# Performance work log

Measured on AMD Instinct MI355X. Metric: run time of the kernel, lower is better.

Reference implementation:

```python
import jax, jax.numpy as jnp
import numpy as np

N, M, B, L, D = 100000, 256, 8, 128, 64
COORD_MAX = 1024


def setup_inputs() -> dict:
    key = jax.random.key(0)
    ks = jax.random.split(key, 9)
    # batch ids sorted so the original loop's centroid_offset == column index
    clu_b = jnp.sort(jax.random.randint(ks[0], (N, 1), 0, B))
    cen_b = jnp.sort(jax.random.randint(ks[1], (M, 1), 0, B))
    clu_xyz = jax.random.randint(ks[2], (N, 3), 0, COORD_MAX)
    cen_xyz = jax.random.randint(ks[3], (M, 3), 0, COORD_MAX)
    return {
        "cluster_coords": jnp.concatenate([clu_b, clu_xyz], axis=1).astype(jnp.int32),
        "centroid_coords": jnp.concatenate([cen_b, cen_xyz], axis=1).astype(jnp.int32),
        "cluster_feats": jax.random.normal(ks[4], (N, L), jnp.float32),
        "centroid_feats": jax.random.normal(ks[5], (M, L), jnp.float32),
        "centroid_conf": jax.random.uniform(ks[6], (M, 1), jnp.float32),
        "W": jax.random.normal(ks[7], (L, D), jnp.float32) * 0.05,
        "b": jax.random.normal(ks[8], (D,), jnp.float32) * 0.05,
    }


def reference(cluster_coords, centroid_coords, cluster_feats, centroid_feats,
              centroid_conf, W, b):
    # pointwise Conv3d(k=1) == linear on features
    clu = cluster_feats @ W + b                      # [N, D]
    nrm = jnp.maximum(jnp.linalg.norm(clu, axis=1, keepdims=True), 1e-12)
    clu = clu / nrm                                  # F.normalize(p=2, dim=1)
    cen = centroid_conf * (centroid_feats @ W + b)   # [M, D]

    # same-batch mask replaces the python loop + scatter
    valid = cluster_coords[:, 0][:, None] == centroid_coords[:, 0][None, :]  # [N, M]

    # pairwise L2 distance on spatial coords via squared expansion (exact for small ints)
    cc = cluster_coords[:, 1:].astype(jnp.float32)   # [N, 3]
    ec = centroid_coords[:, 1:].astype(jnp.float32)  # [M, 3]
    d2 = (jnp.sum(cc * cc, axis=1)[:, None]
          + jnp.sum(ec * ec, axis=1)[None, :]
          - 2.0 * cc @ ec.T)
    dist = jnp.maximum(jnp.sqrt(jnp.maximum(d2, 0.0)), 0.1)  # clamp(min=0.1)

    logits = jnp.where(valid, -dist, -jnp.inf)
    attn = jax.nn.softmax(logits, axis=-1)           # per-row over same-batch centroids
    attn = jnp.where(valid, attn, 0.0)               # rows w/ no centroids -> 0 (matches zeros init)

    out = (clu @ cen.T) * attn                       # [N, M]
    return out
```

## Files before the change

kernel.cpp:

```cpp
#include <hip/hip_runtime.h>
#include <stdint.h>


#define NN 100000
#define MM 256
#define LL 128
#define DD 64
#define NTILES (NN / 16)

typedef float f32x4 __attribute__((ext_vector_type(4)));
typedef __bf16 bf16x8 __attribute__((ext_vector_type(8)));
typedef __fp16 fp16x2 __attribute__((ext_vector_type(2)));

union U16x8 { uint4 u; bf16x8 v; unsigned short s[8]; };
union UH2 { unsigned int u; fp16x2 h; };

static __device__ __forceinline__ unsigned short f2bf(float f) {
  union { float f; unsigned int i; } t; t.f = f;
  unsigned int x = t.i;
  x += 0x7fffu + ((x >> 16) & 1u);
  return (unsigned short)(x >> 16);
}

__global__ __launch_bounds__(256) void prep_kernel(
    const int* __restrict__ cen_coords,
    const float* __restrict__ cen_feats,
    const float* __restrict__ conf,
    const float* __restrict__ W,
    const float* __restrict__ bvec,
    unsigned short* __restrict__ cen_ws,
    unsigned short* __restrict__ wt_ws,
    float4* __restrict__ cmeta_ws)
{
  int tid = threadIdx.x;
  if (blockIdx.x < 16) {
    int m = blockIdx.x * 16 + (tid >> 4);
    int c = tid & 15;
    float a0 = 0.f, a1 = 0.f, a2 = 0.f, a3 = 0.f;
    for (int l = 0; l < LL; l++) {
      float f = cen_feats[m * LL + l];
      const float* wr = W + l * DD + c;
      a0 += f * wr[0];  a1 += f * wr[16];
      a2 += f * wr[32]; a3 += f * wr[48];
    }
    float cf = conf[m];
    cen_ws[m * DD + c +  0] = f2bf(cf * (a0 + bvec[c +  0]));
    cen_ws[m * DD + c + 16] = f2bf(cf * (a1 + bvec[c + 16]));
    cen_ws[m * DD + c + 32] = f2bf(cf * (a2 + bvec[c + 32]));
    cen_ws[m * DD + c + 48] = f2bf(cf * (a3 + bvec[c + 48]));
  } else {
    for (int i = tid; i < LL * DD; i += 256) {
      int l = i >> 6, d = i & 63;
      wt_ws[d * LL + l] = f2bf(W[l * DD + d]);
    }
    {
      int4 cc = ((const int4*)cen_coords)[tid];
      float4 f;
      f.x = (float)cc.y + 4096.0f * (float)cc.x;
      f.y = (float)cc.z;
      f.z = (float)cc.w;
      f.w = 0.0f;
      cmeta_ws[tid] = f;
    }
  }
}

__global__ __launch_bounds__(256, 4) void main_kernel(
    const int4* __restrict__ clu_coords4,
    const float* __restrict__ feats,
    const float* __restrict__ bvec,
    const unsigned short* __restrict__ cen_ws,
    const unsigned short* __restrict__ wt_ws,
    const float4* __restrict__ cmeta,
    float* __restrict__ out)
{
  __shared__ __align__(16) unsigned short clu_s[4][16 * 72];

  int tid = threadIdx.x;
  int wave = tid >> 6, lane = tid & 63;
  int q = lane >> 4, c = lane & 15;
  int tile = blockIdx.x * 4 + wave;
  if (tile >= NTILES) return;

  const float4* fb = (const float4*)(feats + (size_t)(tile * 16 + c) * LL);
  float4 ff[8];
#pragma unroll
  for (int ks = 0; ks < 4; ks++) {
    ff[2 * ks]     = fb[ks * 8 + q * 2];
    ff[2 * ks + 1] = fb[ks * 8 + q * 2 + 1];
  }
  float rx[4], ry[4], rz[4];
#pragma unroll
  for (int r = 0; r < 4; r++) {
    int4 rm = clu_coords4[tile * 16 + q * 4 + r];
    rx[r] = (float)rm.y + 4096.0f * (float)rm.x;
    ry[r] = (float)rm.z;
    rz[r] = (float)rm.w;
  }

  float d2m[4] = {1e30f, 1e30f, 1e30f, 1e30f};
#pragma unroll 4
  for (int mt = 0; mt < 16; mt++) {
    float4 cm = cmeta[mt * 16 + c];
#pragma unroll
    for (int r = 0; r < 4; r++) {
      float dx = rx[r] - cm.x, dy = ry[r] - cm.y, dz = rz[r] - cm.z;
      d2m[r] = fminf(d2m[r], dx * dx + dy * dy + dz * dz);
    }
  }
  float dmv[4];
#pragma unroll
  for (int r = 0; r < 4; r++) {
    d2m[r] = fminf(d2m[r], __shfl_xor(d2m[r], 1));
    d2m[r] = fminf(d2m[r], __shfl_xor(d2m[r], 2));
    d2m[r] = fminf(d2m[r], __shfl_xor(d2m[r], 4));
    d2m[r] = fminf(d2m[r], __shfl_xor(d2m[r], 8));
    dmv[r] = fmaxf(sqrtf(d2m[r]), 0.1f);
  }

  uint2 ep[16];
  float rsum[4] = {0.f, 0.f, 0.f, 0.f};
#pragma unroll
  for (int mt = 0; mt < 16; mt++) {
    float4 cm = cmeta[mt * 16 + c];
    float e[4];
#pragma unroll
    for (int r = 0; r < 4; r++) {
      float dx = rx[r] - cm.x, dy = ry[r] - cm.y, dz = rz[r] - cm.z;
      float d = fmaxf(sqrtf(dx * dx + dy * dy + dz * dz), 0.1f);
      e[r] = __expf(dmv[r] - d);
      rsum[r] += e[r];
    }
    UH2 p0, p1;
    p0.h = __builtin_amdgcn_cvt_pkrtz(e[0], e[1]);
    p1.h = __builtin_amdgcn_cvt_pkrtz(e[2], e[3]);
    ep[mt].x = p0.u;
    ep[mt].y = p1.u;
  }
  float sc[4];
#pragma unroll
  for (int r = 0; r < 4; r++) {
    rsum[r] += __shfl_xor(rsum[r], 1);
    rsum[r] += __shfl_xor(rsum[r], 2);
    rsum[r] += __shfl_xor(rsum[r], 4);
    rsum[r] += __shfl_xor(rsum[r], 8);
    sc[r] = (d2m[r] < 4.0e6f) ? 1.0f / rsum[r] : 0.f;
  }

  f32x4 acc[4] = {{0,0,0,0},{0,0,0,0},{0,0,0,0},{0,0,0,0}};
  {
    const uint4* wb = (const uint4*)wt_ws;
#pragma unroll
    for (int ks = 0; ks < 4; ks++) {
      float4 f0 = ff[2 * ks], f1 = ff[2 * ks + 1];
      U16x8 a;
      a.v[0] = (__bf16)f0.x; a.v[1] = (__bf16)f0.y; a.v[2] = (__bf16)f0.z; a.v[3] = (__bf16)f0.w;
      a.v[4] = (__bf16)f1.x; a.v[5] = (__bf16)f1.y; a.v[6] = (__bf16)f1.z; a.v[7] = (__bf16)f1.w;
#pragma unroll
      for (int nt = 0; nt < 4; nt++) {
        U16x8 b; b.u = wb[(nt * 16 + c) * 16 + ks * 4 + q];
        acc[nt] = __builtin_amdgcn_mfma_f32_16x16x32_bf16(a.v, b.v, acc[nt], 0, 0, 0);
      }
    }
  }
#pragma unroll
  for (int nt = 0; nt < 4; nt++) {
    float bv = bvec[nt * 16 + c];
    acc[nt][0] += bv; acc[nt][1] += bv; acc[nt][2] += bv; acc[nt][3] += bv;
  }
  float inv_nrm[4];
#pragma unroll
  for (int r = 0; r < 4; r++) {
    float s = acc[0][r]*acc[0][r] + acc[1][r]*acc[1][r] + acc[2][r]*acc[2][r] + acc[3][r]*acc[3][r];
    s += __shfl_xor(s, 1); s += __shfl_xor(s, 2); s += __shfl_xor(s, 4); s += __shfl_xor(s, 8);
    inv_nrm[r] = 1.0f / fmaxf(sqrtf(s), 1e-12f);
  }
#pragma unroll
  for (int nt = 0; nt < 4; nt++)
#pragma unroll
    for (int r = 0; r < 4; r++) {
      union { __bf16 h; unsigned short s; } u;
      u.h = (__bf16)(acc[nt][r] * inv_nrm[r]);
      clu_s[wave][(q * 4 + r) * 72 + nt * 16 + c] = u.s;
    }

  __builtin_amdgcn_sched_barrier(0);

  const uint4* cb = (const uint4*)(clu_s[wave]);
  U16x8 a0, a1;
  a0.u = cb[c * 9 + q];
  a1.u = cb[c * 9 + 4 + q];

  const uint4* cenb = (const uint4*)cen_ws;
  float* ob = out + (size_t)(tile * 16 + q * 4) * MM + c;
#pragma unroll
  for (int mt = 0; mt < 16; mt++) {
    U16x8 b0, b1;
    b0.u = cenb[(mt * 16 + c) * 8 + q];
    b1.u = cenb[(mt * 16 + c) * 8 + 4 + q];
    f32x4 dacc = {0, 0, 0, 0};
    dacc = __builtin_amdgcn_mfma_f32_16x16x32_bf16(a0.v, b0.v, dacc, 0, 0, 0);
    dacc = __builtin_amdgcn_mfma_f32_16x16x32_bf16(a1.v, b1.v, dacc, 0, 0, 0);
    UH2 p0, p1; p0.u = ep[mt].x; p1.u = ep[mt].y;
    ob[0 * MM + mt * 16] = dacc[0] * ((float)p0.h[0] * sc[0]);
    ob[1 * MM + mt * 16] = dacc[1] * ((float)p0.h[1] * sc[1]);
    ob[2 * MM + mt * 16] = dacc[2] * ((float)p1.h[0] * sc[2]);
    ob[3 * MM + mt * 16] = dacc[3] * ((float)p1.h[1] * sc[3]);
  }
}

extern "C" void kernel_launch(void* const* d_in, const int* in_sizes, int n_in,
                              void* d_out, int out_size, void* d_ws, size_t ws_size,
                              hipStream_t stream) {
  const int* clu_coords = (const int*)d_in[0];
  const int* cen_coords = (const int*)d_in[1];
  const float* clu_feats = (const float*)d_in[2];
  const float* cen_feats = (const float*)d_in[3];
  const float* conf      = (const float*)d_in[4];
  const float* W         = (const float*)d_in[5];
  const float* bvec      = (const float*)d_in[6];
  float* out = (float*)d_out;

  char* ws = (char*)d_ws;
  unsigned short* cen_ws = (unsigned short*)ws;
  unsigned short* wt_ws  = (unsigned short*)(ws + 32768);
  float4* cmeta_ws       = (float4*)(ws + 32768 + 16384);

  prep_kernel<<<17, 256, 0, stream>>>(cen_coords, cen_feats, conf, W, bvec,
                                      cen_ws, wt_ws, cmeta_ws);
  main_kernel<<<(NTILES + 3) / 4, 256, 0, stream>>>(
      (const int4*)clu_coords, clu_feats, bvec, cen_ws, wt_ws, cmeta_ws, out);
}
```

Measured before the change: 209.0 us.

## Process two row tiles per wave with prefetch and LDS-staged centroid metadata

Each wave now handles two consecutive 16-row tiles. It prefetches the second tile's feature rows right after the first tile's projection MFMAs, so that load overlaps the softmax and output work. Centroid coordinate metadata is staged once per block in shared memory instead of being re-read from global memory in the distance loops. The launch-bounds occupancy hint is dropped and the grid halves, which lowers parallelism and may raise register pressure. Output is written exactly as before.

```diff
diff --git a/kernel.cpp b/kernel.cpp
--- a/kernel.cpp
+++ b/kernel.cpp
@@ -7,6 +7,7 @@
 #define LL 128
 #define DD 64
 #define NTILES (NN / 16)
+#define NJOBS (NTILES / 2)
 
 typedef float f32x4 __attribute__((ext_vector_type(4)));
 typedef __bf16 bf16x8 __attribute__((ext_vector_type(8)));
@@ -65,7 +66,7 @@
   }
 }
 
-__global__ __launch_bounds__(256, 4) void main_kernel(
+__global__ __launch_bounds__(256) void main_kernel(
     const int4* __restrict__ clu_coords4,
     const float* __restrict__ feats,
     const float* __restrict__ bvec,
@@ -75,137 +76,161 @@
     float* __restrict__ out)
 {
   __shared__ __align__(16) unsigned short clu_s[4][16 * 72];
+  __shared__ __align__(16) float4 cmeta_s[MM];
 
   int tid = threadIdx.x;
+  cmeta_s[tid] = cmeta[tid];
+  __syncthreads();
+
   int wave = tid >> 6, lane = tid & 63;
   int q = lane >> 4, c = lane & 15;
-  int tile = blockIdx.x * 4 + wave;
-  if (tile >= NTILES) return;
-
-  const float4* fb = (const float4*)(feats + (size_t)(tile * 16 + c) * LL);
+  int job = blockIdx.x * 4 + wave;
+  if (job >= NJOBS) return;
+  int tile0 = job * 2;
+
+  const float4* fb = (const float4*)(feats + (size_t)(tile0 * 16 + c) * LL);
   float4 ff[8];
 #pragma unroll
   for (int ks = 0; ks < 4; ks++) {
     ff[2 * ks]     = fb[ks * 8 + q * 2];
     ff[2 * ks + 1] = fb[ks * 8 + q * 2 + 1];
   }
-  float rx[4], ry[4], rz[4];
-#pragma unroll
-  for (int r = 0; r < 4; r++) {
-    int4 rm = clu_coords4[tile * 16 + q * 4 + r];
-    rx[r] = (float)rm.y + 4096.0f * (float)rm.x;
-    ry[r] = (float)rm.z;
-    rz[r] = (float)rm.w;
-  }
-
-  float d2m[4] = {1e30f, 1e30f, 1e30f, 1e30f};
+
+#pragma unroll
+  for (int tt = 0; tt < 2; tt++) {
+    int tile = tile0 + tt;
+
+    int4 rm[4];
+#pragma unroll
+    for (int r = 0; r < 4; r++)
+      rm[r] = clu_coords4[tile * 16 + q * 4 + r];
+
+    f32x4 acc[4] = {{0,0,0,0},{0,0,0,0},{0,0,0,0},{0,0,0,0}};
+    {
+      const uint4* wb = (const uint4*)wt_ws;
+#pragma unroll
+      for (int ks = 0; ks < 4; ks++) {
+        float4 f0 = ff[2 * ks], f1 = ff[2 * ks + 1];
+        U16x8 a;
+        a.v[0] = (__bf16)f0.x; a.v[1] = (__bf16)f0.y; a.v[2] = (__bf16)f0.z; a.v[3] = (__bf16)f0.w;
+        a.v[4] = (__bf16)f1.x; a.v[5] = (__bf16)f1.y; a.v[6] = (__bf16)f1.z; a.v[7] = (__bf16)f1.w;
+#pragma unroll
+        for (int nt = 0; nt < 4; nt++) {
+          U16x8 b; b.u = wb[(nt * 16 + c) * 16 + ks * 4 + q];
+          acc[nt] = __builtin_amdgcn_mfma_f32_16x16x32_bf16(a.v, b.v, acc[nt], 0, 0, 0);
+        }
+      }
+    }
+
+    if (tt == 0) {
+#pragma unroll
+      for (int ks = 0; ks < 4; ks++) {
+        ff[2 * ks]     = fb[512 + ks * 8 + q * 2];
+        ff[2 * ks + 1] = fb[512 + ks * 8 + q * 2 + 1];
+      }
+    }
+
+#pragma unroll
+    for (int nt = 0; nt < 4; nt++) {
+      float bv = bvec[nt * 16 + c];
+      acc[nt][0] += bv; acc[nt][1] += bv; acc[nt][2] += bv; acc[nt][3] += bv;
+    }
+    float inv_nrm[4];
+#pragma unroll
+    for (int r = 0; r < 4; r++) {
+      float s = acc[0][r]*acc[0][r] + acc[1][r]*acc[1][r] + acc[2][r]*acc[2][r] + acc[3][r]*acc[3][r];
+      s += __shfl_xor(s, 1); s += __shfl_xor(s, 2); s += __shfl_xor(s, 4); s += __shfl_xor(s, 8);
+      inv_nrm[r] = 1.0f / fmaxf(sqrtf(s), 1e-12f);
+    }
+#pragma unroll
+    for (int nt = 0; nt < 4; nt++)
+#pragma unroll
+      for (int r = 0; r < 4; r++) {
+        union { __bf16 h; unsigned short s; } u;
+        u.h = (__bf16)(acc[nt][r] * inv_nrm[r]);
+        clu_s[wave][(q * 4 + r) * 72 + nt * 16 + c] = u.s;
+      }
+
+    __builtin_amdgcn_sched_barrier(0);
+
+    const uint4* cb = (const uint4*)(clu_s[wave]);
+    U16x8 a0, a1;
+    a0.u = cb[c * 9 + q];
+    a1.u = cb[c * 9 + 4 + q];
+
+    float rx[4], ry[4], rz[4];
+#pragma unroll
+    for (int r = 0; r < 4; r++) {
+      rx[r] = (float)rm[r].y + 4096.0f * (float)rm[r].x;
+      ry[r] = (float)rm[r].z;
+      rz[r] = (float)rm[r].w;
+    }
+
+    float d2m[4] = {1e30f, 1e30f, 1e30f, 1e30f};
 #pragma unroll 4
-  for (int mt = 0; mt < 16; mt++) {
-    float4 cm = cmeta[mt * 16 + c];
-#pragma unroll
-    for (int r = 0; r < 4; r++) {
-      float dx = rx[r] - cm.x, dy = ry[r] - cm.y, dz = rz[r] - cm.z;
-      d2m[r] = fminf(d2m[r], dx * dx + dy * dy + dz * dz);
-    }
-  }
-  float dmv[4];
-#pragma unroll
-  for (int r = 0; r < 4; r++) {
-    d2m[r] = fminf(d2m[r], __shfl_xor(d2m[r], 1));
-    d2m[r] = fminf(d2m[r], __shfl_xor(d2m[r], 2));
-    d2m[r] = fminf(d2m[r], __shfl_xor(d2m[r], 4));
-    d2m[r] = fminf(d2m[r], __shfl_xor(d2m[r], 8));
-    dmv[r] = fmaxf(sqrtf(d2m[r]), 0.1f);
-  }
-
-  uint2 ep[16];
-  float rsum[4] = {0.f, 0.f, 0.f, 0.f};
-#pragma unroll
-  for (int mt = 0; mt < 16; mt++) {
-    float4 cm = cmeta[mt * 16 + c];
-    float e[4];
-#pragma unroll
-    for (int r = 0; r < 4; r++) {
-      float dx = rx[r] - cm.x, dy = ry[r] - cm.y, dz = rz[r] - cm.z;
-      float d = fmaxf(sqrtf(dx * dx + dy * dy + dz * dz), 0.1f);
-      e[r] = __expf(dmv[r] - d);
-      rsum[r] += e[r];
-    }
-    UH2 p0, p1;
-    p0.h = __builtin_amdgcn_cvt_pkrtz(e[0], e[1]);
-    p1.h = __builtin_amdgcn_cvt_pkrtz(e[2], e[3]);
-    ep[mt].x = p0.u;
-    ep[mt].y = p1.u;
-  }
-  float sc[4];
-#pragma unroll
-  for (int r = 0; r < 4; r++) {
-    rsum[r] += __shfl_xor(rsum[r], 1);
-    rsum[r] += __shfl_xor(rsum[r], 2);
-    rsum[r] += __shfl_xor(rsum[r], 4);
-    rsum[r] += __shfl_xor(rsum[r], 8);
-    sc[r] = (d2m[r] < 4.0e6f) ? 1.0f / rsum[r] : 0.f;
-  }
-
-  f32x4 acc[4] = {{0,0,0,0},{0,0,0,0},{0,0,0,0},{0,0,0,0}};
-  {
-    const uint4* wb = (const uint4*)wt_ws;
-#pragma unroll
-    for (int ks = 0; ks < 4; ks++) {
-      float4 f0 = ff[2 * ks], f1 = ff[2 * ks + 1];
-      U16x8 a;
-      a.v[0] = (__bf16)f0.x; a.v[1] = (__bf16)f0.y; a.v[2] = (__bf16)f0.z; a.v[3] = (__bf16)f0.w;
-      a.v[4] = (__bf16)f1.x; a.v[5] = (__bf16)f1.y; a.v[6] = (__bf16)f1.z; a.v[7] = (__bf16)f1.w;
-#pragma unroll
-      for (int nt = 0; nt < 4; nt++) {
-        U16x8 b; b.u = wb[(nt * 16 + c) * 16 + ks * 4 + q];
-        acc[nt] = __builtin_amdgcn_mfma_f32_16x16x32_bf16(a.v, b.v, acc[nt], 0, 0, 0);
-      }
-    }
-  }
-#pragma unroll
-  for (int nt = 0; nt < 4; nt++) {
-    float bv = bvec[nt * 16 + c];
-    acc[nt][0] += bv; acc[nt][1] += bv; acc[nt][2] += bv; acc[nt][3] += bv;
-  }
-  float inv_nrm[4];
-#pragma unroll
-  for (int r = 0; r < 4; r++) {
-    float s = acc[0][r]*acc[0][r] + acc[1][r]*acc[1][r] + acc[2][r]*acc[2][r] + acc[3][r]*acc[3][r];
-    s += __shfl_xor(s, 1); s += __shfl_xor(s, 2); s += __shfl_xor(s, 4); s += __shfl_xor(s, 8);
-    inv_nrm[r] = 1.0f / fmaxf(sqrtf(s), 1e-12f);
-  }
-#pragma unroll
-  for (int nt = 0; nt < 4; nt++)
-#pragma unroll
-    for (int r = 0; r < 4; r++) {
-      union { __bf16 h; unsigned short s; } u;
-      u.h = (__bf16)(acc[nt][r] * inv_nrm[r]);
-      clu_s[wave][(q * 4 + r) * 72 + nt * 16 + c] = u.s;
-    }
-
-  __builtin_amdgcn_sched_barrier(0);
-
-  const uint4* cb = (const uint4*)(clu_s[wave]);
-  U16x8 a0, a1;
-  a0.u = cb[c * 9 + q];
-  a1.u = cb[c * 9 + 4 + q];
-
-  const uint4* cenb = (const uint4*)cen_ws;
-  float* ob = out + (size_t)(tile * 16 + q * 4) * MM + c;
-#pragma unroll
-  for (int mt = 0; mt < 16; mt++) {
-    U16x8 b0, b1;
-    b0.u = cenb[(mt * 16 + c) * 8 + q];
-    b1.u = cenb[(mt * 16 + c) * 8 + 4 + q];
-    f32x4 dacc = {0, 0, 0, 0};
-    dacc = __builtin_amdgcn_mfma_f32_16x16x32_bf16(a0.v, b0.v, dacc, 0, 0, 0);
-    dacc = __builtin_amdgcn_mfma_f32_16x16x32_bf16(a1.v, b1.v, dacc, 0, 0, 0);
-    UH2 p0, p1; p0.u = ep[mt].x; p1.u = ep[mt].y;
-    ob[0 * MM + mt * 16] = dacc[0] * ((float)p0.h[0] * sc[0]);
-    ob[1 * MM + mt * 16] = dacc[1] * ((float)p0.h[1] * sc[1]);
-    ob[2 * MM + mt * 16] = dacc[2] * ((float)p1.h[0] * sc[2]);
-    ob[3 * MM + mt * 16] = dacc[3] * ((float)p1.h[1] * sc[3]);
+    for (int mt = 0; mt < 16; mt++) {
+      float4 cm = cmeta_s[mt * 16 + c];
+#pragma unroll
+      for (int r = 0; r < 4; r++) {
+        float dx = rx[r] - cm.x, dy = ry[r] - cm.y, dz = rz[r] - cm.z;
+        d2m[r] = fminf(d2m[r], dx * dx + dy * dy + dz * dz);
+      }
+    }
+    float dmv[4];
+#pragma unroll
+    for (int r = 0; r < 4; r++) {
+      d2m[r] = fminf(d2m[r], __shfl_xor(d2m[r], 1));
+      d2m[r] = fminf(d2m[r], __shfl_xor(d2m[r], 2));
+      d2m[r] = fminf(d2m[r], __shfl_xor(d2m[r], 4));
+      d2m[r] = fminf(d2m[r], __shfl_xor(d2m[r], 8));
+      dmv[r] = fmaxf(sqrtf(d2m[r]), 0.1f);
+    }
+
+    uint2 ep[16];
+    float rsum[4] = {0.f, 0.f, 0.f, 0.f};
+#pragma unroll
+    for (int mt = 0; mt < 16; mt++) {
+      float4 cm = cmeta_s[mt * 16 + c];
+      float e[4];
+#pragma unroll
+      for (int r = 0; r < 4; r++) {
+        float dx = rx[r] - cm.x, dy = ry[r] - cm.y, dz = rz[r] - cm.z;
+        float d = fmaxf(sqrtf(dx * dx + dy * dy + dz * dz), 0.1f);
+        e[r] = __expf(dmv[r] - d);
+        rsum[r] += e[r];
+      }
+      UH2 p0, p1;
+      p0.h = __builtin_amdgcn_cvt_pkrtz(e[0], e[1]);
+      p1.h = __builtin_amdgcn_cvt_pkrtz(e[2], e[3]);
+      ep[mt].x = p0.u;
+      ep[mt].y = p1.u;
+    }
+    float sc[4];
+#pragma unroll
+    for (int r = 0; r < 4; r++) {
+      rsum[r] += __shfl_xor(rsum[r], 1);
+      rsum[r] += __shfl_xor(rsum[r], 2);
+      rsum[r] += __shfl_xor(rsum[r], 4);
+      rsum[r] += __shfl_xor(rsum[r], 8);
+      sc[r] = (d2m[r] < 4.0e6f) ? 1.0f / rsum[r] : 0.f;
+    }
+
+    const uint4* cenb = (const uint4*)cen_ws;
+    float* ob = out + (size_t)(tile * 16 + q * 4) * MM + c;
+#pragma unroll
+    for (int mt = 0; mt < 16; mt++) {
+      U16x8 b0, b1;
+      b0.u = cenb[(mt * 16 + c) * 8 + q];
+      b1.u = cenb[(mt * 16 + c) * 8 + 4 + q];
+      f32x4 dacc = {0, 0, 0, 0};
+      dacc = __builtin_amdgcn_mfma_f32_16x16x32_bf16(a0.v, b0.v, dacc, 0, 0, 0);
+      dacc = __builtin_amdgcn_mfma_f32_16x16x32_bf16(a1.v, b1.v, dacc, 0, 0, 0);
+      UH2 p0, p1; p0.u = ep[mt].x; p1.u = ep[mt].y;
+      ob[0 * MM + mt * 16] = dacc[0] * ((float)p0.h[0] * sc[0]);
+      ob[1 * MM + mt * 16] = dacc[1] * ((float)p0.h[1] * sc[1]);
+      ob[2 * MM + mt * 16] = dacc[2] * ((float)p1.h[0] * sc[2]);
+      ob[3 * MM + mt * 16] = dacc[3] * ((float)p1.h[1] * sc[3]);
+    }
   }
 }
 
@@ -228,6 +253,6 @@
 
   prep_kernel<<<17, 256, 0, stream>>>(cen_coords, cen_feats, conf, W, bvec,
                                       cen_ws, wt_ws, cmeta_ws);
-  main_kernel<<<(NTILES + 3) / 4, 256, 0, stream>>>(
+  main_kernel<<<(NJOBS + 3) / 4, 256, 0, stream>>>(
       (const int4*)clu_coords, clu_feats, bvec, cen_ws, wt_ws, cmeta_ws, out);
 }
```

Measured after the change: 202.6 us. 1.03x faster.

## Transpose MFMA output mapping for float4 row stores and stage centroid meta in LDS

Applied to the files above, without the earlier changes.

Swaps the MFMA operand order so each lane holds four consecutive centroid columns of a single cluster row. This turns the output writes into float4 stores, and the attention math becomes one row per lane, reducing shuffles and per-row state. Centroid metadata is staged once into shared memory with a block barrier, and the linear/normalize stage is moved ahead of the distance computation. Occupancy hint is raised from 4 to 5 blocks per CU, which may cause register spills.

```diff
diff --git a/kernel.cpp b/kernel.cpp
--- a/kernel.cpp
+++ b/kernel.cpp
@@ -65,7 +65,7 @@
   }
 }
 
-__global__ __launch_bounds__(256, 4) void main_kernel(
+__global__ __launch_bounds__(256, 5) void main_kernel(
     const int4* __restrict__ clu_coords4,
     const float* __restrict__ feats,
     const float* __restrict__ bvec,
@@ -75,8 +75,12 @@
     float* __restrict__ out)
 {
   __shared__ __align__(16) unsigned short clu_s[4][16 * 72];
+  __shared__ __align__(16) float4 cmeta_s[MM];
 
   int tid = threadIdx.x;
+  cmeta_s[tid] = cmeta[tid];
+  __syncthreads();
+
   int wave = tid >> 6, lane = tid & 63;
   int q = lane >> 4, c = lane & 15;
   int tile = blockIdx.x * 4 + wave;
@@ -89,47 +93,81 @@
     ff[2 * ks]     = fb[ks * 8 + q * 2];
     ff[2 * ks + 1] = fb[ks * 8 + q * 2 + 1];
   }
-  float rx[4], ry[4], rz[4];
+  int4 rm = clu_coords4[tile * 16 + c];
+  float rx = (float)rm.y + 4096.0f * (float)rm.x;
+  float ry = (float)rm.z;
+  float rz = (float)rm.w;
+
+  f32x4 acc[4] = {{0,0,0,0},{0,0,0,0},{0,0,0,0},{0,0,0,0}};
+  {
+    const uint4* wb = (const uint4*)wt_ws;
+#pragma unroll
+    for (int ks = 0; ks < 4; ks++) {
+      float4 f0 = ff[2 * ks], f1 = ff[2 * ks + 1];
+      U16x8 a;
+      a.v[0] = (__bf16)f0.x; a.v[1] = (__bf16)f0.y; a.v[2] = (__bf16)f0.z; a.v[3] = (__bf16)f0.w;
+      a.v[4] = (__bf16)f1.x; a.v[5] = (__bf16)f1.y; a.v[6] = (__bf16)f1.z; a.v[7] = (__bf16)f1.w;
+#pragma unroll
+      for (int nt = 0; nt < 4; nt++) {
+        U16x8 b; b.u = wb[(nt * 16 + c) * 16 + ks * 4 + q];
+        acc[nt] = __builtin_amdgcn_mfma_f32_16x16x32_bf16(a.v, b.v, acc[nt], 0, 0, 0);
+      }
+    }
+  }
+#pragma unroll
+  for (int nt = 0; nt < 4; nt++) {
+    float bv = bvec[nt * 16 + c];
+    acc[nt][0] += bv; acc[nt][1] += bv; acc[nt][2] += bv; acc[nt][3] += bv;
+  }
+  float inv_nrm[4];
 #pragma unroll
   for (int r = 0; r < 4; r++) {
-    int4 rm = clu_coords4[tile * 16 + q * 4 + r];
-    rx[r] = (float)rm.y + 4096.0f * (float)rm.x;
-    ry[r] = (float)rm.z;
-    rz[r] = (float)rm.w;
-  }
-
-  float d2m[4] = {1e30f, 1e30f, 1e30f, 1e30f};
-#pragma unroll 4
+    float s = acc[0][r]*acc[0][r] + acc[1][r]*acc[1][r] + acc[2][r]*acc[2][r] + acc[3][r]*acc[3][r];
+    s += __shfl_xor(s, 1); s += __shfl_xor(s, 2); s += __shfl_xor(s, 4); s += __shfl_xor(s, 8);
+    inv_nrm[r] = 1.0f / fmaxf(sqrtf(s), 1e-12f);
+  }
+#pragma unroll
+  for (int nt = 0; nt < 4; nt++)
+#pragma unroll
+    for (int r = 0; r < 4; r++) {
+      union { __bf16 h; unsigned short s; } u;
+      u.h = (__bf16)(acc[nt][r] * inv_nrm[r]);
+      clu_s[wave][(q * 4 + r) * 72 + nt * 16 + c] = u.s;
+    }
+
+  __builtin_amdgcn_sched_barrier(0);
+
+  const uint4* cb = (const uint4*)(clu_s[wave]);
+  U16x8 a0, a1;
+  a0.u = cb[c * 9 + q];
+  a1.u = cb[c * 9 + 4 + q];
+
+  float d2m = 1e30f;
+#pragma unroll
   for (int mt = 0; mt < 16; mt++) {
-    float4 cm = cmeta[mt * 16 + c];
 #pragma unroll
     for (int r = 0; r < 4; r++) {
-      float dx = rx[r] - cm.x, dy = ry[r] - cm.y, dz = rz[r] - cm.z;
-      d2m[r] = fminf(d2m[r], dx * dx + dy * dy + dz * dz);
-    }
-  }
-  float dmv[4];
-#pragma unroll
-  for (int r = 0; r < 4; r++) {
-    d2m[r] = fminf(d2m[r], __shfl_xor(d2m[r], 1));
-    d2m[r] = fminf(d2m[r], __shfl_xor(d2m[r], 2));
-    d2m[r] = fminf(d2m[r], __shfl_xor(d2m[r], 4));
-    d2m[r] = fminf(d2m[r], __shfl_xor(d2m[r], 8));
-    dmv[r] = fmaxf(sqrtf(d2m[r]), 0.1f);
-  }
+      float4 cm = cmeta_s[mt * 16 + q * 4 + r];
+      float dx = rx - cm.x, dy = ry - cm.y, dz = rz - cm.z;
+      d2m = fminf(d2m, dx * dx + dy * dy + dz * dz);
+    }
+  }
+  d2m = fminf(d2m, __shfl_xor(d2m, 16));
+  d2m = fminf(d2m, __shfl_xor(d2m, 32));
+  float dmv = fmaxf(sqrtf(d2m), 0.1f);
 
   uint2 ep[16];
-  float rsum[4] = {0.f, 0.f, 0.f, 0.f};
+  float rsum = 0.f;
 #pragma unroll
   for (int mt = 0; mt < 16; mt++) {
-    float4 cm = cmeta[mt * 16 + c];
     float e[4];
 #pragma unroll
     for (int r = 0; r < 4; r++) {
-      float dx = rx[r] - cm.x, dy = ry[r] - cm.y, dz = rz[r] - cm.z;
+      float4 cm = cmeta_s[mt * 16 + q * 4 + r];
+      float dx = rx - cm.x, dy = ry - cm.y, dz = rz - cm.z;
       float d = fmaxf(sqrtf(dx * dx + dy * dy + dz * dz), 0.1f);
-      e[r] = __expf(dmv[r] - d);
-      rsum[r] += e[r];
+      e[r] = __expf(dmv - d);
+      rsum += e[r];
     }
     UH2 p0, p1;
     p0.h = __builtin_amdgcn_cvt_pkrtz(e[0], e[1]);
@@ -137,75 +175,27 @@
     ep[mt].x = p0.u;
     ep[mt].y = p1.u;
   }
-  float sc[4];
-#pragma unroll
-  for (int r = 0; r < 4; r++) {
-    rsum[r] += __shfl_xor(rsum[r], 1);
-    rsum[r] += __shfl_xor(rsum[r], 2);
-    rsum[r] += __shfl_xor(rsum[r], 4);
-    rsum[r] += __shfl_xor(rsum[r], 8);
-    sc[r] = (d2m[r] < 4.0e6f) ? 1.0f / rsum[r] : 0.f;
-  }
-
-  f32x4 acc[4] = {{0,0,0,0},{0,0,0,0},{0,0,0,0},{0,0,0,0}};
-  {
-    const uint4* wb = (const uint4*)wt_ws;
-#pragma unroll
-    for (int ks = 0; ks < 4; ks++) {
-      float4 f0 = ff[2 * ks], f1 = ff[2 * ks + 1];
-      U16x8 a;
-      a.v[0] = (__bf16)f0.x; a.v[1] = (__bf16)f0.y; a.v[2] = (__bf16)f0.z; a.v[3] = (__bf16)f0.w;
-      a.v[4] = (__bf16)f1.x; a.v[5] = (__bf16)f1.y; a.v[6] = (__bf16)f1.z; a.v[7] = (__bf16)f1.w;
-#pragma unroll
-      for (int nt = 0; nt < 4; nt++) {
-        U16x8 b; b.u = wb[(nt * 16 + c) * 16 + ks * 4 + q];
-        acc[nt] = __builtin_amdgcn_mfma_f32_16x16x32_bf16(a.v, b.v, acc[nt], 0, 0, 0);
-      }
-    }
-  }
-#pragma unroll
-  for (int nt = 0; nt < 4; nt++) {
-    float bv = bvec[nt * 16 + c];
-    acc[nt][0] += bv; acc[nt][1] += bv; acc[nt][2] += bv; acc[nt][3] += bv;
-  }
-  float inv_nrm[4];
-#pragma unroll
-  for (int r = 0; r < 4; r++) {
-    float s = acc[0][r]*acc[0][r] + acc[1][r]*acc[1][r] + acc[2][r]*acc[2][r] + acc[3][r]*acc[3][r];
-    s += __shfl_xor(s, 1); s += __shfl_xor(s, 2); s += __shfl_xor(s, 4); s += __shfl_xor(s, 8);
-    inv_nrm[r] = 1.0f / fmaxf(sqrtf(s), 1e-12f);
-  }
-#pragma unroll
-  for (int nt = 0; nt < 4; nt++)
-#pragma unroll
-    for (int r = 0; r < 4; r++) {
-      union { __bf16 h; unsigned short s; } u;
-      u.h = (__bf16)(acc[nt][r] * inv_nrm[r]);
-      clu_s[wave][(q * 4 + r) * 72 + nt * 16 + c] = u.s;
-    }
-
-  __builtin_amdgcn_sched_barrier(0);
-
-  const uint4* cb = (const uint4*)(clu_s[wave]);
-  U16x8 a0, a1;
-  a0.u = cb[c * 9 + q];
-  a1.u = cb[c * 9 + 4 + q];
+  rsum += __shfl_xor(rsum, 16);
+  rsum += __shfl_xor(rsum, 32);
+  float sc = (d2m < 4.0e6f) ? 1.0f / rsum : 0.f;
 
   const uint4* cenb = (const uint4*)cen_ws;
-  float* ob = out + (size_t)(tile * 16 + q * 4) * MM + c;
+  float4* ob4 = (float4*)(out + (size_t)(tile * 16 + c) * MM) + q;
 #pragma unroll
   for (int mt = 0; mt < 16; mt++) {
     U16x8 b0, b1;
     b0.u = cenb[(mt * 16 + c) * 8 + q];
     b1.u = cenb[(mt * 16 + c) * 8 + 4 + q];
     f32x4 dacc = {0, 0, 0, 0};
-    dacc = __builtin_amdgcn_mfma_f32_16x16x32_bf16(a0.v, b0.v, dacc, 0, 0, 0);
-    dacc = __builtin_amdgcn_mfma_f32_16x16x32_bf16(a1.v, b1.v, dacc, 0, 0, 0);
+    dacc = __builtin_amdgcn_mfma_f32_16x16x32_bf16(b0.v, a0.v, dacc, 0, 0, 0);
+    dacc = __builtin_amdgcn_mfma_f32_16x16x32_bf16(b1.v, a1.v, dacc, 0, 0, 0);
     UH2 p0, p1; p0.u = ep[mt].x; p1.u = ep[mt].y;
-    ob[0 * MM + mt * 16] = dacc[0] * ((float)p0.h[0] * sc[0]);
-    ob[1 * MM + mt * 16] = dacc[1] * ((float)p0.h[1] * sc[1]);
-    ob[2 * MM + mt * 16] = dacc[2] * ((float)p1.h[0] * sc[2]);
-    ob[3 * MM + mt * 16] = dacc[3] * ((float)p1.h[1] * sc[3]);
+    float4 v;
+    v.x = dacc[0] * ((float)p0.h[0] * sc);
+    v.y = dacc[1] * ((float)p0.h[1] * sc);
+    v.z = dacc[2] * ((float)p1.h[0] * sc);
+    v.w = dacc[3] * ((float)p1.h[1] * sc);
+    ob4[mt * 4] = v;
   }
 }
 
```

Result: faster. 200.7 us (-4.0%).
